# Kernel optimization log

Hardware: AMD Instinct MI355X
Metric: run time of the kernel (lower is better)

Reference implementation:

```python
import jax, jax.numpy as jnp
import numpy as np

SIZE = 4096


def fast_hadamard_transform(x, normalize=True):
    """Walsh-Hadamard transform along last dim via log2(n) butterfly stages."""
    orig_shape = x.shape
    n = orig_shape[-1]
    h = 1
    while h < n:
        # view as (..., n//(2h), 2, h) and butterfly the pair axis
        x = x.reshape(orig_shape[:-1] + (n // (2 * h), 2, h))
        a = x[..., 0, :]
        b = x[..., 1, :]
        x = jnp.stack([a + b, a - b], axis=-2).reshape(orig_shape)
        h *= 2
    if normalize:
        x = x * (1.0 / np.sqrt(n)).astype(x.dtype)
    return x


def setup_inputs() -> dict:
    key = jax.random.key(0)
    kx, ks, kb = jax.random.split(key, 3)
    x = jax.random.normal(kx, (4, 4096, SIZE), dtype=jnp.float32)
    # adaptive_init: scale ~ N(1.0, 0.1), shift ~ N(0.0, 0.01)
    scale = 1.0 + 0.1 * jax.random.normal(ks, (SIZE,), dtype=jnp.float32)
    shift = 0.01 * jax.random.normal(kb, (SIZE,), dtype=jnp.float32)
    return {"x": x, "scale": scale, "shift": shift}


def reference(x, scale, shift):
    x_h = fast_hadamard_transform(x, normalize=True)
    return scale * x_h + shift
```

## Files before the change

kernel.cpp:

```cpp
#include <hip/hip_runtime.h>


#define ROW 4096
#define STR 17

__device__ __forceinline__ void wht16(float v[16]) {
#pragma unroll
  for (int h = 1; h < 16; h <<= 1) {
#pragma unroll
    for (int i = 0; i < 16; ++i) {
      if ((i & h) == 0) {
        float a = v[i], b = v[i | h];
        v[i] = a + b;
        v[i | h] = a - b;
      }
    }
  }
}

__global__ __launch_bounds__(256) void AdaptiveHadamardTransform_kernel(
    const float* __restrict__ x, const float* __restrict__ scale,
    const float* __restrict__ shift, float* __restrict__ out) {
  __shared__ float lds[256 * STR];

  const int t = threadIdx.x;
  const long long base = (long long)blockIdx.x * ROW;

  float v[16];

  const float4* __restrict__ x4 = reinterpret_cast<const float4*>(x + base + 16 * t);
#pragma unroll
  for (int j = 0; j < 4; ++j) {
    const float4 f = x4[j];
    v[4 * j + 0] = f.x;
    v[4 * j + 1] = f.y;
    v[4 * j + 2] = f.z;
    v[4 * j + 3] = f.w;
  }
  wht16(v);

#pragma unroll
  for (int j = 0; j < 16; ++j) lds[t * STR + j] = v[j];
  __syncthreads();

  {
    const int i2 = t >> 4, i0 = t & 15;
#pragma unroll
    for (int r = 0; r < 16; ++r) v[r] = lds[(i2 * 16 + r) * STR + i0];
    wht16(v);
#pragma unroll
    for (int r = 0; r < 16; ++r) lds[(i2 * 16 + r) * STR + i0] = v[r];
  }
  __syncthreads();

  {
    const int i1 = t >> 4, i0 = t & 15;
#pragma unroll
    for (int r = 0; r < 16; ++r) v[r] = lds[(r * 16 + i1) * STR + i0];
  }
  wht16(v);

  const float norm = 0.015625f;
#pragma unroll
  for (int r = 0; r < 16; ++r) {
    const int c = r * 256 + t;
    const float o = fmaf(scale[c], v[r] * norm, shift[c]);
    __builtin_nontemporal_store(o, out + base + c);
  }
}

extern "C" void kernel_launch(void* const* d_in, const int* in_sizes, int n_in,
                              void* d_out, int out_size, void* d_ws, size_t ws_size,
                              hipStream_t stream) {
  const float* x = (const float*)d_in[0];
  const float* scale = (const float*)d_in[1];
  const float* shift = (const float*)d_in[2];
  float* out = (float*)d_out;

  const int rows = in_sizes[0] / ROW;
  AdaptiveHadamardTransform_kernel<<<rows, 256, 0, stream>>>(x, scale, shift, out);
}
```

Measured before the change: 441.3 us.

## Restructure Hadamard to 64x64 decomposition with one wavefront per row

Replaces the three-stage 16x16x16 radix decomposition (256 threads, two LDS transposes) with a 64x64 decomposition. Each of 64 lanes holds 64 values, so a row needs only one LDS transpose and one barrier. Loads become strided per-lane scalar nontemporal loads, and stores become per-lane float4 writes of contiguous 64-element chunks. The cost is heavy register pressure (64 floats per lane plus butterflies), less vectorized loads, and strided store coalescing across lanes.

```diff
diff --git a/kernel.cpp b/kernel.cpp
--- a/kernel.cpp
+++ b/kernel.cpp
@@ -2,15 +2,17 @@
 
 
 #define ROW 4096
-#define STR 17
+#define PAD 65
 
-__device__ __forceinline__ void wht16(float v[16]) {
+typedef float floatx4 __attribute__((ext_vector_type(4)));
+
+__device__ __forceinline__ void wht64(float v[64]) {
 #pragma unroll
-  for (int h = 1; h < 16; h <<= 1) {
+  for (int h = 1; h < 64; h <<= 1) {
 #pragma unroll
-    for (int i = 0; i < 16; ++i) {
+    for (int i = 0; i < 64; ++i) {
       if ((i & h) == 0) {
-        float a = v[i], b = v[i | h];
+        const float a = v[i], b = v[i | h];
         v[i] = a + b;
         v[i | h] = a - b;
       }
@@ -18,54 +20,45 @@
   }
 }
 
-__global__ __launch_bounds__(256) void AdaptiveHadamardTransform_kernel(
+__global__ __launch_bounds__(64) void AdaptiveHadamardTransform_kernel(
     const float* __restrict__ x, const float* __restrict__ scale,
     const float* __restrict__ shift, float* __restrict__ out) {
-  __shared__ float lds[256 * STR];
+  __shared__ float lds[64 * PAD];
 
-  const int t = threadIdx.x;
+  const int l = threadIdx.x;
   const long long base = (long long)blockIdx.x * ROW;
 
-  float v[16];
+  float v[64];
 
-  const float4* __restrict__ x4 = reinterpret_cast<const float4*>(x + base + 16 * t);
+  const float* __restrict__ xr = x + base + l;
 #pragma unroll
-  for (int j = 0; j < 4; ++j) {
-    const float4 f = x4[j];
-    v[4 * j + 0] = f.x;
-    v[4 * j + 1] = f.y;
-    v[4 * j + 2] = f.z;
-    v[4 * j + 3] = f.w;
-  }
-  wht16(v);
+  for (int h = 0; h < 64; ++h)
+    v[h] = __builtin_nontemporal_load(xr + 64 * h);
+
+  wht64(v);
 
 #pragma unroll
-  for (int j = 0; j < 16; ++j) lds[t * STR + j] = v[j];
+  for (int h = 0; h < 64; ++h) lds[l * PAD + h] = v[h];
   __syncthreads();
+#pragma unroll
+  for (int j = 0; j < 64; ++j) v[j] = lds[j * PAD + l];
 
-  {
-    const int i2 = t >> 4, i0 = t & 15;
-#pragma unroll
-    for (int r = 0; r < 16; ++r) v[r] = lds[(i2 * 16 + r) * STR + i0];
-    wht16(v);
-#pragma unroll
-    for (int r = 0; r < 16; ++r) lds[(i2 * 16 + r) * STR + i0] = v[r];
-  }
-  __syncthreads();
-
-  {
-    const int i1 = t >> 4, i0 = t & 15;
-#pragma unroll
-    for (int r = 0; r < 16; ++r) v[r] = lds[(r * 16 + i1) * STR + i0];
-  }
-  wht16(v);
+  wht64(v);
 
   const float norm = 0.015625f;
+  const floatx4* __restrict__ s4 = reinterpret_cast<const floatx4*>(scale + 64 * l);
+  const floatx4* __restrict__ h4 = reinterpret_cast<const floatx4*>(shift + 64 * l);
+  floatx4* __restrict__ o4 = reinterpret_cast<floatx4*>(out + base + 64 * l);
 #pragma unroll
-  for (int r = 0; r < 16; ++r) {
-    const int c = r * 256 + t;
-    const float o = fmaf(scale[c], v[r] * norm, shift[c]);
-    __builtin_nontemporal_store(o, out + base + c);
+  for (int j = 0; j < 16; ++j) {
+    const floatx4 sc = s4[j];
+    const floatx4 sh = h4[j];
+    floatx4 o;
+    o.x = fmaf(sc.x, v[4 * j + 0] * norm, sh.x);
+    o.y = fmaf(sc.y, v[4 * j + 1] * norm, sh.y);
+    o.z = fmaf(sc.z, v[4 * j + 2] * norm, sh.z);
+    o.w = fmaf(sc.w, v[4 * j + 3] * norm, sh.w);
+    __builtin_nontemporal_store(o, o4 + j);
   }
 }
 
@@ -78,5 +71,5 @@
   float* out = (float*)d_out;
 
   const int rows = in_sizes[0] / ROW;
-  AdaptiveHadamardTransform_kernel<<<rows, 256, 0, stream>>>(x, scale, shift, out);
+  AdaptiveHadamardTransform_kernel<<<rows, 64, 0, stream>>>(x, scale, shift, out);
 }
```

Result: slower. 1.037 ms (+135.0%).

## Process multiple rows per block with register prefetch of next row

Applied to the files above, without the earlier changes.

Each block now processes 8 rows in a loop instead of one. While the current row goes through the LDS transpose stages, the next row's input is prefetched into registers, so global load latency overlaps with compute. The grid shrinks by 8x, which reduces launch parallelism and adds an extra barrier per row, and the extra prefetch registers raise register pressure.

```diff
diff --git a/kernel.cpp b/kernel.cpp
--- a/kernel.cpp
+++ b/kernel.cpp
@@ -3,6 +3,7 @@
 
 #define ROW 4096
 #define STR 17
+#define RPB 8
 
 __device__ __forceinline__ void wht16(float v[16]) {
 #pragma unroll
@@ -24,48 +25,74 @@
   __shared__ float lds[256 * STR];
 
   const int t = threadIdx.x;
-  const long long base = (long long)blockIdx.x * ROW;
+  const long long row0 = (long long)blockIdx.x * RPB;
 
-  float v[16];
+  float v[16], nxt[16];
 
-  const float4* __restrict__ x4 = reinterpret_cast<const float4*>(x + base + 16 * t);
+  {
+    const float4* __restrict__ x4 =
+        reinterpret_cast<const float4*>(x + row0 * ROW + 16 * t);
 #pragma unroll
-  for (int j = 0; j < 4; ++j) {
-    const float4 f = x4[j];
-    v[4 * j + 0] = f.x;
-    v[4 * j + 1] = f.y;
-    v[4 * j + 2] = f.z;
-    v[4 * j + 3] = f.w;
+    for (int j = 0; j < 4; ++j) {
+      const float4 f = x4[j];
+      v[4 * j + 0] = f.x;
+      v[4 * j + 1] = f.y;
+      v[4 * j + 2] = f.z;
+      v[4 * j + 3] = f.w;
+    }
   }
-  wht16(v);
+
+  for (int rr = 0; rr < RPB; ++rr) {
+    const long long base = (row0 + rr) * ROW;
+
+    wht16(v);
+
+    if (rr + 1 < RPB) {
+      const float4* __restrict__ x4 =
+          reinterpret_cast<const float4*>(x + (base + ROW) + 16 * t);
+#pragma unroll
+      for (int j = 0; j < 4; ++j) {
+        const float4 f = x4[j];
+        nxt[4 * j + 0] = f.x;
+        nxt[4 * j + 1] = f.y;
+        nxt[4 * j + 2] = f.z;
+        nxt[4 * j + 3] = f.w;
+      }
+    }
 
 #pragma unroll
-  for (int j = 0; j < 16; ++j) lds[t * STR + j] = v[j];
-  __syncthreads();
+    for (int j = 0; j < 16; ++j) lds[t * STR + j] = v[j];
+    __syncthreads();
 
-  {
-    const int i2 = t >> 4, i0 = t & 15;
+    {
+      const int i2 = t >> 4, i0 = t & 15;
 #pragma unroll
-    for (int r = 0; r < 16; ++r) v[r] = lds[(i2 * 16 + r) * STR + i0];
+      for (int r = 0; r < 16; ++r) v[r] = lds[(i2 * 16 + r) * STR + i0];
+      wht16(v);
+#pragma unroll
+      for (int r = 0; r < 16; ++r) lds[(i2 * 16 + r) * STR + i0] = v[r];
+    }
+    __syncthreads();
+
+    {
+      const int i1 = t >> 4, i0 = t & 15;
+#pragma unroll
+      for (int r = 0; r < 16; ++r) v[r] = lds[(r * 16 + i1) * STR + i0];
+    }
     wht16(v);
+
+    const float norm = 0.015625f;
 #pragma unroll
-    for (int r = 0; r < 16; ++r) lds[(i2 * 16 + r) * STR + i0] = v[r];
-  }
-  __syncthreads();
+    for (int r = 0; r < 16; ++r) {
+      const int c = r * 256 + t;
+      const float o = fmaf(scale[c], v[r] * norm, shift[c]);
+      __builtin_nontemporal_store(o, out + base + c);
+    }
 
-  {
-    const int i1 = t >> 4, i0 = t & 15;
+    __syncthreads();
+
 #pragma unroll
-    for (int r = 0; r < 16; ++r) v[r] = lds[(r * 16 + i1) * STR + i0];
-  }
-  wht16(v);
-
-  const float norm = 0.015625f;
-#pragma unroll
-  for (int r = 0; r < 16; ++r) {
-    const int c = r * 256 + t;
-    const float o = fmaf(scale[c], v[r] * norm, shift[c]);
-    __builtin_nontemporal_store(o, out + base + c);
+    for (int j = 0; j < 16; ++j) v[j] = nxt[j];
   }
 }
 
@@ -78,5 +105,5 @@
   float* out = (float*)d_out;
 
   const int rows = in_sizes[0] / ROW;
-  AdaptiveHadamardTransform_kernel<<<rows, 256, 0, stream>>>(x, scale, shift, out);
+  AdaptiveHadamardTransform_kernel<<<rows / RPB, 256, 0, stream>>>(x, scale, shift, out);
 }
```

Result: slower. 455.6 us (+3.2%).

## Process multiple rows per block with async LDS prefetch of next row

Applied to the files above, without the earlier changes.

Each block now handles eight rows and prefetches the next row directly into LDS with global_load_lds while the current row's butterfly stages run. Scale and shift are loaded once per block into registers, and output is written with float4 stores instead of scalar nontemporal stores. The LDS layout for the transposes is reorganized with new padding strides. This trades fewer, larger blocks and more LDS per block for overlap of global loads with compute.

```diff
diff --git a/kernel.cpp b/kernel.cpp
--- a/kernel.cpp
+++ b/kernel.cpp
@@ -2,7 +2,10 @@
 
 
 #define ROW 4096
-#define STR 17
+#define NT 256
+#define RPB 8
+#define S2 277
+#define SI1 17
 
 __device__ __forceinline__ void wht16(float v[16]) {
 #pragma unroll
@@ -18,54 +21,102 @@
   }
 }
 
-__global__ __launch_bounds__(256) void AdaptiveHadamardTransform_kernel(
+__device__ __forceinline__ void glld16(const float* g, float* l) {
+  __builtin_amdgcn_global_load_lds(
+      (const __attribute__((address_space(1))) void*)g,
+      (__attribute__((address_space(3))) void*)l, 16, 0, 0);
+}
+
+#define WAIT_VM(N)                                      \
+  asm volatile("s_waitcnt vmcnt(" #N ")" ::: "memory"); \
+  __builtin_amdgcn_sched_barrier(0)
+#define WAIT_LGKM                                     \
+  asm volatile("s_waitcnt lgkmcnt(0)" ::: "memory"); \
+  __builtin_amdgcn_sched_barrier(0)
+#define BAR asm volatile("s_barrier" ::: "memory")
+
+__global__ __launch_bounds__(NT, 4) void AdaptiveHadamardTransform_kernel(
     const float* __restrict__ x, const float* __restrict__ scale,
     const float* __restrict__ shift, float* __restrict__ out) {
-  __shared__ float lds[256 * STR];
+  __shared__ float stage[ROW];
+  __shared__ float work[16 * S2];
 
   const int t = threadIdx.x;
-  const long long base = (long long)blockIdx.x * ROW;
+  const int wid = t >> 6, lane = t & 63;
+  const long long row0 = (long long)blockIdx.x * RPB;
+
+  float4 sc[4], sh[4];
+  {
+    const float4* s4 = reinterpret_cast<const float4*>(scale + 16 * t);
+    const float4* h4 = reinterpret_cast<const float4*>(shift + 16 * t);
+#pragma unroll
+    for (int q = 0; q < 4; ++q) {
+      sc[q] = s4[q];
+      sh[q] = h4[q];
+    }
+  }
+
+  const int c1 = SI1 * (t >> 4) + (t & 15);
+  const int c2 = S2 * (t >> 4) + (t & 15);
+  const int c3 = S2 * (t >> 4) + SI1 * (t & 15);
+
+  {
+    const float* g = x + row0 * ROW;
+#pragma unroll
+    for (int q = 0; q < 4; ++q)
+      glld16(g + (wid * 4 + q) * 256 + lane * 4, &stage[(wid * 4 + q) * 256]);
+  }
+  WAIT_VM(0);
+  BAR;
 
   float v[16];
+  const float norm = 0.015625f;
 
-  const float4* __restrict__ x4 = reinterpret_cast<const float4*>(x + base + 16 * t);
-#pragma unroll
-  for (int j = 0; j < 4; ++j) {
-    const float4 f = x4[j];
-    v[4 * j + 0] = f.x;
-    v[4 * j + 1] = f.y;
-    v[4 * j + 2] = f.z;
-    v[4 * j + 3] = f.w;
-  }
-  wht16(v);
+  for (int r = 0; r < RPB; ++r) {
+    const long long base = (row0 + r) * ROW;
+
+    if (r) {
+      WAIT_VM(4);
+      BAR;
+    }
 
 #pragma unroll
-  for (int j = 0; j < 16; ++j) lds[t * STR + j] = v[j];
-  __syncthreads();
-
-  {
-    const int i2 = t >> 4, i0 = t & 15;
-#pragma unroll
-    for (int r = 0; r < 16; ++r) v[r] = lds[(i2 * 16 + r) * STR + i0];
+    for (int k = 0; k < 16; ++k) v[k] = stage[t + 256 * k];
     wht16(v);
 #pragma unroll
-    for (int r = 0; r < 16; ++r) lds[(i2 * 16 + r) * STR + i0] = v[r];
-  }
-  __syncthreads();
+    for (int k = 0; k < 16; ++k) work[S2 * k + c1] = v[k];
+    WAIT_LGKM;
+    BAR;
 
-  {
-    const int i1 = t >> 4, i0 = t & 15;
+    if (r + 1 < RPB) {
+      const float* g = x + base + ROW;
 #pragma unroll
-    for (int r = 0; r < 16; ++r) v[r] = lds[(r * 16 + i1) * STR + i0];
-  }
-  wht16(v);
+      for (int q = 0; q < 4; ++q)
+        glld16(g + (wid * 4 + q) * 256 + lane * 4, &stage[(wid * 4 + q) * 256]);
+    }
 
-  const float norm = 0.015625f;
 #pragma unroll
-  for (int r = 0; r < 16; ++r) {
-    const int c = r * 256 + t;
-    const float o = fmaf(scale[c], v[r] * norm, shift[c]);
-    __builtin_nontemporal_store(o, out + base + c);
+    for (int k = 0; k < 16; ++k) v[k] = work[c2 + SI1 * k];
+    wht16(v);
+#pragma unroll
+    for (int k = 0; k < 16; ++k) work[c2 + SI1 * k] = v[k];
+    WAIT_LGKM;
+    BAR;
+
+#pragma unroll
+    for (int j = 0; j < 16; ++j) v[j] = work[c3 + j];
+    wht16(v);
+
+    float4* o4 = reinterpret_cast<float4*>(out + base + 16 * t);
+#pragma unroll
+    for (int q = 0; q < 4; ++q) {
+      float4 o;
+      o.x = fmaf(sc[q].x, v[4 * q + 0] * norm, sh[q].x);
+      o.y = fmaf(sc[q].y, v[4 * q + 1] * norm, sh[q].y);
+      o.z = fmaf(sc[q].z, v[4 * q + 2] * norm, sh[q].z);
+      o.w = fmaf(sc[q].w, v[4 * q + 3] * norm, sh[q].w);
+      o4[q] = o;
+    }
   }
 }
 
@@ -78,5 +129,5 @@
   float* out = (float*)d_out;
 
   const int rows = in_sizes[0] / ROW;
-  AdaptiveHadamardTransform_kernel<<<rows, 256, 0, stream>>>(x, scale, shift, out);
+  AdaptiveHadamardTransform_kernel<<<rows / RPB, NT, 0, stream>>>(x, scale, shift, out);
 }
```

Result: slower. 450.6 us (+2.1%).
